# Kernel optimization log

Hardware: AMD Instinct MI355X
Metric: run time of the kernel (lower is better)

## Reference

```python
import jax, jax.numpy as jnp
import numpy as np

W_SEG = 2048   # segment length w
R = 4          # dilation rate
OFFSET = 0     # offset < r
H = 16         # num heads
C = 1024       # embed dim
M = W_SEG // R # tokens attended per segment


def _mha(xi, w_in, b_in, w_out, b_out):
    # xi: (b, s, m, c) -> causal multi-head self-attention per segment
    b, s, m, c = xi.shape
    dh = c // H
    qkv = jnp.einsum('bsmc,ec->bsme', xi, w_in) + b_in  # e = 3c
    q, k, v = jnp.split(qkv, 3, axis=-1)
    q = q.reshape(b, s, m, H, dh)
    k = k.reshape(b, s, m, H, dh)
    v = v.reshape(b, s, m, H, dh)
    scores = jnp.einsum('bsqhd,bskhd->bshqk', q, k) / jnp.sqrt(jnp.asarray(dh, xi.dtype))
    causal = jnp.tril(jnp.ones((m, m), dtype=bool))
    scores = jnp.where(causal, scores, jnp.asarray(-1e9, xi.dtype))
    p = jax.nn.softmax(scores, axis=-1)
    o = jnp.einsum('bshqk,bskhd->bsqhd', p, v).reshape(b, s, m, c)
    return jnp.einsum('bsmc,oc->bsmo', o, w_out) + b_out


def setup_inputs() -> dict:
    key = jax.random.key(0)
    k1, k2, k3, k4, k5 = jax.random.split(key, 5)
    x = jax.random.normal(k1, (4, 8192, C), dtype=jnp.float32)
    w_in = jax.random.normal(k2, (3 * C, C), dtype=jnp.float32) * (C ** -0.5)
    b_in = jnp.zeros((3 * C,), dtype=jnp.float32)
    w_out = jax.random.normal(k3, (C, C), dtype=jnp.float32) * (C ** -0.5)
    b_out = jnp.zeros((C,), dtype=jnp.float32)
    return {"x": x, "w_in": w_in, "b_in": b_in, "w_out": w_out, "b_out": b_out}


def reference(x, w_in, b_in, w_out, b_out):
    b, n, c = x.shape
    s = n // W_SEG  # number of segments
    xr = x.reshape(b, s, W_SEG, c)
    xi = xr[:, :, OFFSET::R, :]                # (b, s, m, c) dilated gather
    oi = _mha(xi, w_in, b_in, w_out, b_out)    # attention per segment
    out = jnp.zeros_like(xr).at[:, :, OFFSET::R, :].set(oi)  # scatter (disjoint indices)
    return out.reshape(b, n, c)
```

## Files before the change

kernel.cpp:

```cpp
#include <hip/hip_runtime.h>


typedef unsigned short u16;
typedef short short8 __attribute__((ext_vector_type(8)));
typedef float f32x4 __attribute__((ext_vector_type(4)));

__device__ __forceinline__ u16 f2bf(float f) {
  unsigned u = __builtin_bit_cast(unsigned, f);
  u += 0x7FFFu + ((u >> 16) & 1u);
  return (u16)(u >> 16);
}

__device__ __forceinline__ void gload_lds16(const void* g, void* l) {
  __builtin_amdgcn_global_load_lds((const __attribute__((address_space(1))) void*)g,
                                   (__attribute__((address_space(3))) void*)l,
                                   16, 0, 0);
}

#define SBAR() asm volatile("s_barrier" ::: "memory")

__global__ void conv_gather(const float* __restrict__ x, u16* __restrict__ xi) {
  int t = blockIdx.x * 256 + threadIdx.x;
  if (t >= (8192 * 1024) / 8) return;
  int row = t >> 7;
  int col = (t & 127) << 3;
  size_t src = ((size_t)((row >> 9) << 11) + ((row & 511) << 2)) * 1024 + col;
  float4 v0 = *(const float4*)(x + src);
  float4 v1 = *(const float4*)(x + src + 4);
  short8 o;
  o[0] = f2bf(v0.x); o[1] = f2bf(v0.y); o[2] = f2bf(v0.z); o[3] = f2bf(v0.w);
  o[4] = f2bf(v1.x); o[5] = f2bf(v1.y); o[6] = f2bf(v1.z); o[7] = f2bf(v1.w);
  *(short8*)(xi + (size_t)row * 1024 + col) = o;
}

__global__ void conv_plain(const float* __restrict__ in, u16* __restrict__ out, int n8) {
  int t = blockIdx.x * 256 + threadIdx.x;
  if (t >= n8) return;
  size_t base = (size_t)t * 8;
  float4 v0 = *(const float4*)(in + base);
  float4 v1 = *(const float4*)(in + base + 4);
  short8 o;
  o[0] = f2bf(v0.x); o[1] = f2bf(v0.y); o[2] = f2bf(v0.z); o[3] = f2bf(v0.w);
  o[4] = f2bf(v1.x); o[5] = f2bf(v1.y); o[6] = f2bf(v1.z); o[7] = f2bf(v1.w);
  *(short8*)(out + base) = o;
}

__global__ __launch_bounds__(512) void gemm_qkv8(
    const u16* __restrict__ A, const u16* __restrict__ B,
    const float* __restrict__ bias, u16* __restrict__ C) {
  constexpr int K = 1024, N = 3072, NT = 16;
  __shared__ u16 lds[3][24576];

  const int tid = threadIdx.x;
  const int w = tid >> 6, lane = tid & 63;
  const int wm = w >> 2, wn = w & 3;
  const int g = lane >> 4, lq = lane & 15;

  const int s = (blockIdx.x & 7) * 96 + (blockIdx.x >> 3);
  const int m0 = (s / 12) * 128, n0 = (s % 12) * 256;

  const int srow = w * 8 + (lane >> 3);
  const int jch = (lane & 7) ^ ((lane >> 3) & 7);
  const u16* Ab = A + (size_t)(m0 + srow) * K + jch * 8;
  const u16* Bb = B + (size_t)(n0 + srow) * K + jch * 8;
  const int ldst = w * 512 + lane * 8;

#define SA(buf_, qd, kt) gload_lds16(Ab + (size_t)(qd) * 64 * K + (kt) * 64, &lds[buf_][(qd) * 4096 + ldst])
#define SB(buf_, qd, kt) gload_lds16(Bb + (size_t)(qd) * 64 * K + (kt) * 64, &lds[buf_][8192 + (qd) * 4096 + ldst])

  const int xw = lq & 7;
  const int arow = wm * 64 + lq;
  const int brow = wn * 64 + lq;

#define RDA(kc)                                                                   \
  _Pragma("unroll") for (int mi = 0; mi < 4; ++mi)                                \
      af[mi] = *(const short8*)(&lds[buf][(arow + mi * 16) * 64 + (((kc) * 4 + g) ^ xw) * 8]);
#define RDB(kc)                                                                   \
  _Pragma("unroll") for (int ni = 0; ni < 4; ++ni)                                \
      bf[ni] = *(const short8*)(&lds[buf][8192 + (brow + ni * 16) * 64 + (((kc) * 4 + g) ^ xw) * 8]);
#define MFMA16()                                                                  \
  __builtin_amdgcn_s_setprio(1);                                                  \
  _Pragma("unroll") for (int mi = 0; mi < 4; ++mi)                                \
      _Pragma("unroll") for (int ni = 0; ni < 4; ++ni)                            \
          acc[mi][ni] = __builtin_amdgcn_mfma_f32_16x16x32_bf16(                  \
              af[mi], bf[ni], acc[mi][ni], 0, 0, 0);                              \
  __builtin_amdgcn_s_setprio(0);

  f32x4 acc[4][4] = {};

  SA(0, 0, 0); SA(0, 1, 0); SB(0, 0, 0); SB(0, 1, 0); SB(0, 2, 0); SB(0, 3, 0);
  SA(1, 0, 1); SA(1, 1, 1); SB(1, 0, 1); SB(1, 1, 1); SB(1, 2, 1); SB(1, 3, 1);
  asm volatile("s_waitcnt vmcnt(6)" ::: "memory");
  SBAR();

#pragma unroll 1
  for (int t = 0; t < NT; ++t) {
    const int buf = t % 3, nb = (t + 2) % 3;
    short8 af[4], bf[4];

    if (t + 2 < NT) { SA(nb, 0, t + 2); SA(nb, 1, t + 2); SB(nb, 0, t + 2); }
    RDA(0); RDB(0);
    SBAR();
    MFMA16();
    SBAR();

    if (t + 2 < NT) { SB(nb, 1, t + 2); SB(nb, 2, t + 2); SB(nb, 3, t + 2); }
    RDA(1); RDB(1);
    if (t + 2 < NT) { asm volatile("s_waitcnt vmcnt(6)" ::: "memory"); }
    else            { asm volatile("s_waitcnt vmcnt(0)" ::: "memory"); }
    SBAR();
    MFMA16();
    SBAR();
  }

#pragma unroll
  for (int mi = 0; mi < 4; ++mi) {
#pragma unroll
    for (int ni = 0; ni < 4; ++ni) {
      const int col = n0 + wn * 64 + ni * 16 + lq;
      const float bv = bias[col];
#pragma unroll
      for (int r = 0; r < 4; ++r) {
        const int m = m0 + wm * 64 + mi * 16 + g * 4 + r;
        C[(size_t)m * N + col] = f2bf(acc[mi][ni][r] + bv);
      }
    }
  }
#undef SA
#undef SB
#undef RDA
#undef RDB
#undef MFMA16
}

__global__ __launch_bounds__(256) void gemm_out(
    const u16* __restrict__ A, const u16* __restrict__ B,
    const float* __restrict__ bias, float* __restrict__ Cout,
    int M, int N, int K) {
  __shared__ u16 As[128 * 32];
  __shared__ u16 Bs[128 * 32];
  const int tid = threadIdx.x;
  const int w = tid >> 6, lane = tid & 63;
  const int wr = w >> 1, wc = w & 1;
  const int g = lane >> 4, lq = lane & 15;
  const int m0 = blockIdx.x * 128, n0 = blockIdx.y * 128;
  const int sr = w * 16 + (lane >> 2);
  const int sc = (lane & 3) * 8;
  f32x4 acc[4][4] = {};

  for (int k0 = 0; k0 < K; k0 += 32) {
    gload_lds16(A + (size_t)(m0 + sr) * K + k0 + sc,      &As[sr * 32 + sc]);
    gload_lds16(A + (size_t)(m0 + 64 + sr) * K + k0 + sc, &As[(64 + sr) * 32 + sc]);
    gload_lds16(B + (size_t)(n0 + sr) * K + k0 + sc,      &Bs[sr * 32 + sc]);
    gload_lds16(B + (size_t)(n0 + 64 + sr) * K + k0 + sc, &Bs[(64 + sr) * 32 + sc]);
    __syncthreads();

    short8 af[4], bf[4];
#pragma unroll
    for (int i = 0; i < 4; ++i) {
      af[i] = *reinterpret_cast<const short8*>(&As[(wr * 64 + i * 16 + lq) * 32 + g * 8]);
      bf[i] = *reinterpret_cast<const short8*>(&Bs[(wc * 64 + i * 16 + lq) * 32 + g * 8]);
    }
#pragma unroll
    for (int mi = 0; mi < 4; ++mi)
#pragma unroll
      for (int ni = 0; ni < 4; ++ni)
        acc[mi][ni] = __builtin_amdgcn_mfma_f32_16x16x32_bf16(af[mi], bf[ni], acc[mi][ni], 0, 0, 0);
    __syncthreads();
  }

#pragma unroll
  for (int mi = 0; mi < 4; ++mi) {
#pragma unroll
    for (int ni = 0; ni < 4; ++ni) {
      const int col = n0 + wc * 64 + ni * 16 + lq;
      const float bv = bias[col];
#pragma unroll
      for (int r = 0; r < 4; ++r) {
        const int m = m0 + wr * 64 + mi * 16 + g * 4 + r;
        const float v = acc[mi][ni][r] + bv;
        const int orow = ((m >> 9) << 11) + ((m & 511) << 2);
        float* o = Cout + (size_t)orow * 1024 + col;
        o[0] = v;
        o[1024] = 0.f;
        o[2048] = 0.f;
        o[3072] = 0.f;
      }
    }
  }
}

__global__ __launch_bounds__(256) void transpose_v(const u16* __restrict__ qkv,
                                                   u16* __restrict__ vt) {
  __shared__ u16 T[128][72];
  const int bh = blockIdx.x, kb = blockIdx.y * 128;
  const int bs = bh >> 4, h = bh & 15;
  const int tid = threadIdx.x;
  const u16* src = qkv + (size_t)(bs * 512 + kb) * 3072 + 2048 + h * 64;
#pragma unroll
  for (int i = 0; i < 4; ++i) {
    int s = tid + i * 256;
    int r = s >> 3, cc = s & 7;
    int pc = cc ^ ((r >> 3) & 7);
    *reinterpret_cast<short8*>(&T[r][pc * 8]) =
        *reinterpret_cast<const short8*>(src + (size_t)r * 3072 + cc * 8);
  }
  __syncthreads();
  u16* dst = vt + (size_t)bh * 64 * 512 + kb;
#pragma unroll
  for (int i = 0; i < 4; ++i) {
    int s = tid + i * 256;
    int d = s >> 4, m = s & 15;
    short8 o;
#pragma unroll
    for (int j = 0; j < 8; ++j) {
      int r = m * 8 + j;
      o[j] = T[r][(((d >> 3) ^ ((r >> 3) & 7)) << 3) + (d & 7)];
    }
    *reinterpret_cast<short8*>(dst + (size_t)d * 512 + m * 8) = o;
  }
}

__global__ __launch_bounds__(512) void attn_kernel(const u16* __restrict__ qkv,
                                                   const u16* __restrict__ vt,
                                                   u16* __restrict__ o_ws) {
  __shared__ u16 Ks[512 * 64];
  __shared__ u16 Vs[64 * 512];
  __shared__ u16 Pl[8][16][40];

  const int tid = threadIdx.x;
  const int w = tid >> 6, lane = tid & 63;
  const int g = lane >> 4, lq = lane & 15;
  const int bh = blockIdx.x;
  const int bs = bh >> 4, h = bh & 15;

  const u16* baseq = qkv + (size_t)bs * 512 * 3072 + h * 64;
  const u16* basek = baseq + 1024;
  const u16* vhead = vt + (size_t)bh * 64 * 512;

  {
    const int rsub = lane >> 3;
    const int csw = (lane & 7) ^ rsub;
#pragma unroll
    for (int i = 0; i < 8; ++i) {
      const int step = i * 8 + w;
      gload_lds16(basek + (size_t)(step * 8 + rsub) * 3072 + csw * 8,
                  &Ks[step * 512 + lane * 8]);
    }
#pragma unroll
    for (int i = 0; i < 8; ++i) {
      const int d = i * 8 + w;
      gload_lds16(vhead + (size_t)d * 512 + (lane ^ (d & 7)) * 8,
                  &Vs[d * 512 + lane * 8]);
    }
  }
  __syncthreads();

  const int xw = lq & 7;
#pragma unroll 1
  for (int qi = 0; qi < 4; ++qi) {
    const int qt = ((qi & 1) ? (15 - w) : w) + (qi >> 1) * 16;
    const int q0 = qt * 16;
    const short8 qf0 = *(const short8*)(baseq + (size_t)(q0 + lq) * 3072 + g * 8);
    const short8 qf1 = *(const short8*)(baseq + (size_t)(q0 + lq) * 3072 + 32 + g * 8);
    f32x4 oacc[4] = {};
    float l_r[4] = {0.f, 0.f, 0.f, 0.f};
    const int nst = (qt + 2) >> 1;
#pragma unroll 1
    for (int kk = 0; kk < nst; ++kk) {
      const int kb = kk * 32;
      const bool last = (kk == nst - 1);
      f32x4 s[2];
#pragma unroll
      for (int tt = 0; tt < 2; ++tt) {
        const int r = kb + tt * 16 + lq;
        short8 klo = *(const short8*)(&Ks[r * 64 + ((g ^ xw) * 8)]);
        short8 khi = *(const short8*)(&Ks[r * 64 + (((4 + g) ^ xw) * 8)]);
        f32x4 z = {};
        z = __builtin_amdgcn_mfma_f32_16x16x32_bf16(qf0, klo, z, 0, 0, 0);
        z = __builtin_amdgcn_mfma_f32_16x16x32_bf16(qf1, khi, z, 0, 0, 0);
        s[tt] = z;
      }
#pragma unroll
      for (int tt = 0; tt < 2; ++tt) {
#pragma unroll
        for (int r = 0; r < 4; ++r) {
          float p = __expf(s[tt][r] * 0.125f);
          if (last && (kb + tt * 16 + lq > q0 + g * 4 + r)) p = 0.f;
          l_r[r] += p;
          Pl[w][g * 4 + r][tt * 16 + lq] = f2bf(p);
        }
      }
      short8 pf = *(const short8*)(&Pl[w][lq][g * 8]);
#pragma unroll
      for (int dt = 0; dt < 4; ++dt) {
        const int vr = dt * 16 + lq;
        short8 vf = *(const short8*)(&Vs[vr * 512 + ((((kb >> 3) + g) ^ xw) * 8)]);
        oacc[dt] = __builtin_amdgcn_mfma_f32_16x16x32_bf16(pf, vf, oacc[dt], 0, 0, 0);
      }
    }
#pragma unroll
    for (int r = 0; r < 4; ++r) {
      float l = l_r[r];
      l += __shfl_xor(l, 1);
      l += __shfl_xor(l, 2);
      l += __shfl_xor(l, 4);
      l += __shfl_xor(l, 8);
      const float inv = 1.0f / l;
      const int q = q0 + g * 4 + r;
      u16* dst = o_ws + (size_t)(bs * 512 + q) * 1024 + h * 64;
#pragma unroll
      for (int dt = 0; dt < 4; ++dt) dst[dt * 16 + lq] = f2bf(oacc[dt][r] * inv);
    }
  }
}

extern "C" void kernel_launch(void* const* d_in, const int* in_sizes, int n_in,
                              void* d_out, int out_size, void* d_ws, size_t ws_size,
                              hipStream_t stream) {
  const float* x     = (const float*)d_in[0];
  const float* w_in  = (const float*)d_in[1];
  const float* b_in  = (const float*)d_in[2];
  const float* w_out = (const float*)d_in[3];
  const float* b_out = (const float*)d_in[4];

  char* ws = (char*)d_ws;
  u16* vt      = (u16*)(ws);
  u16* xi_bf   = (u16*)(ws);
  u16* win_bf  = (u16*)(ws + 16777216);
  u16* wout_bf = (u16*)(ws + 16777216 + 6291456);
  u16* qkv     = (u16*)(ws + 16777216 + 6291456 + 2097152);
  u16* o_bf    = (u16*)(ws + 16777216 + 6291456 + 2097152 + 50331648);

  conv_gather<<<4096, 256, 0, stream>>>(x, xi_bf);
  conv_plain<<<1536, 256, 0, stream>>>(w_in, win_bf, (3072 * 1024) / 8);
  conv_plain<<<512, 256, 0, stream>>>(w_out, wout_bf, (1024 * 1024) / 8);
  gemm_qkv8<<<768, 512, 0, stream>>>(xi_bf, win_bf, b_in, qkv);
  transpose_v<<<dim3(256, 4), 256, 0, stream>>>(qkv, vt);
  attn_kernel<<<256, 512, 0, stream>>>(qkv, vt, o_bf);
  gemm_out<<<dim3(64, 8), 256, 0, stream>>>(o_bf, wout_bf, b_out, (float*)d_out, 8192, 1024, 1024);
}
```

Baseline: 161.4 us.

## Fuse V transpose into QKV GEMM epilogue and vectorize zero-fill

The QKV GEMM epilogue now writes Q and K into separate planar buffers and V directly in transposed per-head layout, so the separate transpose kernel and its extra read/write pass go away. The attention kernel's addressing is updated to match. The output GEMM replaces its scalar zero stores for the dilated gaps with a coalesced float4 fill loop. The V epilogue stores are 8-byte strided writes, which may coalesce less well.

New measurement: 155.4 us. -3.8%, faster.

```diff
diff --git a/kernel.cpp b/kernel.cpp
--- a/kernel.cpp
+++ b/kernel.cpp
@@ -3,6 +3,7 @@
 
 typedef unsigned short u16;
 typedef short short8 __attribute__((ext_vector_type(8)));
+typedef short short4v __attribute__((ext_vector_type(4)));
 typedef float f32x4 __attribute__((ext_vector_type(4)));
 
 __device__ __forceinline__ u16 f2bf(float f) {
@@ -48,7 +49,7 @@
 __global__ __launch_bounds__(512) void gemm_qkv8(
     const u16* __restrict__ A, const u16* __restrict__ B,
     const float* __restrict__ bias, u16* __restrict__ C) {
-  constexpr int K = 1024, N = 3072, NT = 16;
+  constexpr int K = 1024, NT = 16;
   __shared__ u16 lds[3][24576];
 
   const int tid = threadIdx.x;
@@ -113,16 +114,36 @@
     SBAR();
   }
 
-#pragma unroll
-  for (int mi = 0; mi < 4; ++mi) {
-#pragma unroll
-    for (int ni = 0; ni < 4; ++ni) {
-      const int col = n0 + wn * 64 + ni * 16 + lq;
-      const float bv = bias[col];
-#pragma unroll
-      for (int r = 0; r < 4; ++r) {
-        const int m = m0 + wm * 64 + mi * 16 + g * 4 + r;
-        C[(size_t)m * N + col] = f2bf(acc[mi][ni][r] + bv);
+  if (n0 < 2048) {
+#pragma unroll
+    for (int mi = 0; mi < 4; ++mi) {
+#pragma unroll
+      for (int ni = 0; ni < 4; ++ni) {
+        const int col = n0 + wn * 64 + ni * 16 + lq;
+        const float bv = bias[col];
+        u16* dst = C + (size_t)(col >> 10) * 8388608 + (col & 1023);
+#pragma unroll
+        for (int r = 0; r < 4; ++r) {
+          const int m = m0 + wm * 64 + mi * 16 + g * 4 + r;
+          dst[(size_t)m * 1024] = f2bf(acc[mi][ni][r] + bv);
+        }
+      }
+    }
+  } else {
+    u16* vt = C + 16777216;
+#pragma unroll
+    for (int mi = 0; mi < 4; ++mi) {
+      const int m4 = m0 + wm * 64 + mi * 16 + g * 4;
+      const int bs = m4 >> 9, k = m4 & 511;
+#pragma unroll
+      for (int ni = 0; ni < 4; ++ni) {
+        const int cv = n0 - 2048 + wn * 64 + ni * 16 + lq;
+        const int h = cv >> 6, d = cv & 63;
+        const float bv = bias[cv + 2048];
+        short4v pk;
+#pragma unroll
+        for (int r = 0; r < 4; ++r) pk[r] = (short)f2bf(acc[mi][ni][r] + bv);
+        *(short4v*)(&vt[(size_t)((bs * 16 + h) * 64 + d) * 512 + k]) = pk;
       }
     }
   }
@@ -178,51 +199,25 @@
 #pragma unroll
       for (int r = 0; r < 4; ++r) {
         const int m = m0 + wr * 64 + mi * 16 + g * 4 + r;
-        const float v = acc[mi][ni][r] + bv;
         const int orow = ((m >> 9) << 11) + ((m & 511) << 2);
-        float* o = Cout + (size_t)orow * 1024 + col;
-        o[0] = v;
-        o[1024] = 0.f;
-        o[2048] = 0.f;
-        o[3072] = 0.f;
-      }
-    }
-  }
-}
-
-__global__ __launch_bounds__(256) void transpose_v(const u16* __restrict__ qkv,
-                                                   u16* __restrict__ vt) {
-  __shared__ u16 T[128][72];
-  const int bh = blockIdx.x, kb = blockIdx.y * 128;
-  const int bs = bh >> 4, h = bh & 15;
-  const int tid = threadIdx.x;
-  const u16* src = qkv + (size_t)(bs * 512 + kb) * 3072 + 2048 + h * 64;
-#pragma unroll
-  for (int i = 0; i < 4; ++i) {
-    int s = tid + i * 256;
-    int r = s >> 3, cc = s & 7;
-    int pc = cc ^ ((r >> 3) & 7);
-    *reinterpret_cast<short8*>(&T[r][pc * 8]) =
-        *reinterpret_cast<const short8*>(src + (size_t)r * 3072 + cc * 8);
-  }
-  __syncthreads();
-  u16* dst = vt + (size_t)bh * 64 * 512 + kb;
-#pragma unroll
-  for (int i = 0; i < 4; ++i) {
-    int s = tid + i * 256;
-    int d = s >> 4, m = s & 15;
-    short8 o;
-#pragma unroll
-    for (int j = 0; j < 8; ++j) {
-      int r = m * 8 + j;
-      o[j] = T[r][(((d >> 3) ^ ((r >> 3) & 7)) << 3) + (d & 7)];
-    }
-    *reinterpret_cast<short8*>(dst + (size_t)d * 512 + m * 8) = o;
+        Cout[(size_t)orow * 1024 + col] = acc[mi][ni][r] + bv;
+      }
+    }
+  }
+
+  for (int i = 0; i < 48; ++i) {
+    const int idx = i * 256 + tid;
+    const int z = idx >> 12;
+    const int mm = (idx & 4095) >> 5;
+    const int ch = idx & 31;
+    const int m = m0 + mm;
+    const int orow = ((m >> 9) << 11) + ((m & 511) << 2) + 1 + z;
+    *(float4*)(Cout + (size_t)orow * 1024 + n0 + ch * 4) =
+        make_float4(0.f, 0.f, 0.f, 0.f);
   }
 }
 
 __global__ __launch_bounds__(512) void attn_kernel(const u16* __restrict__ qkv,
-                                                   const u16* __restrict__ vt,
                                                    u16* __restrict__ o_ws) {
   __shared__ u16 Ks[512 * 64];
   __shared__ u16 Vs[64 * 512];
@@ -234,9 +229,9 @@
   const int bh = blockIdx.x;
   const int bs = bh >> 4, h = bh & 15;
 
-  const u16* baseq = qkv + (size_t)bs * 512 * 3072 + h * 64;
-  const u16* basek = baseq + 1024;
-  const u16* vhead = vt + (size_t)bh * 64 * 512;
+  const u16* baseq = qkv + (size_t)bs * 512 * 1024 + h * 64;
+  const u16* basek = qkv + 8388608 + (size_t)bs * 512 * 1024 + h * 64;
+  const u16* vhead = qkv + 16777216 + (size_t)bh * 32768;
 
   {
     const int rsub = lane >> 3;
@@ -244,7 +239,7 @@
 #pragma unroll
     for (int i = 0; i < 8; ++i) {
       const int step = i * 8 + w;
-      gload_lds16(basek + (size_t)(step * 8 + rsub) * 3072 + csw * 8,
+      gload_lds16(basek + (size_t)(step * 8 + rsub) * 1024 + csw * 8,
                   &Ks[step * 512 + lane * 8]);
     }
 #pragma unroll
@@ -261,8 +256,8 @@
   for (int qi = 0; qi < 4; ++qi) {
     const int qt = ((qi & 1) ? (15 - w) : w) + (qi >> 1) * 16;
     const int q0 = qt * 16;
-    const short8 qf0 = *(const short8*)(baseq + (size_t)(q0 + lq) * 3072 + g * 8);
-    const short8 qf1 = *(const short8*)(baseq + (size_t)(q0 + lq) * 3072 + 32 + g * 8);
+    const short8 qf0 = *(const short8*)(baseq + (size_t)(q0 + lq) * 1024 + g * 8);
+    const short8 qf1 = *(const short8*)(baseq + (size_t)(q0 + lq) * 1024 + 32 + g * 8);
     f32x4 oacc[4] = {};
     float l_r[4] = {0.f, 0.f, 0.f, 0.f};
     const int nst = (qt + 2) >> 1;
@@ -325,7 +320,6 @@
   const float* b_out = (const float*)d_in[4];
 
   char* ws = (char*)d_ws;
-  u16* vt      = (u16*)(ws);
   u16* xi_bf   = (u16*)(ws);
   u16* win_bf  = (u16*)(ws + 16777216);
   u16* wout_bf = (u16*)(ws + 16777216 + 6291456);
@@ -336,7 +330,6 @@
   conv_plain<<<1536, 256, 0, stream>>>(w_in, win_bf, (3072 * 1024) / 8);
   conv_plain<<<512, 256, 0, stream>>>(w_out, wout_bf, (1024 * 1024) / 8);
   gemm_qkv8<<<768, 512, 0, stream>>>(xi_bf, win_bf, b_in, qkv);
-  transpose_v<<<dim3(256, 4), 256, 0, stream>>>(qkv, vt);
-  attn_kernel<<<256, 512, 0, stream>>>(qkv, vt, o_bf);
+  attn_kernel<<<256, 512, 0, stream>>>(qkv, o_bf);
   gemm_out<<<dim3(64, 8), 256, 0, stream>>>(o_bf, wout_bf, b_out, (float*)d_out, 8192, 1024, 1024);
 }
```
